# Optimization experiments

Hardware: AMD Instinct MI355X
Metric: run time of the kernel (lower is better)

The kernel has to match this reference:

```python
import jax, jax.numpy as jnp
import numpy as np

DIM = 2048
NUM_HEADS = 16
NUM_KV_HEADS = 4
HEAD_DIM = DIM // NUM_HEADS  # 128
ROPE_DIMS = HEAD_DIM         # rope_dims=0 -> full head_dim
ROPE_BASE = 10000.0
EPS = jnp.finfo(jnp.float32).eps  # torch F.rms_norm default eps


def _rms_norm(x):
    # F.rms_norm over last dim, no learned weight
    return x * jax.lax.rsqrt(jnp.mean(x * x, axis=-1, keepdims=True) + EPS)


def _rope_cos_sin(seq_len, dtype):
    inv_freq = 1.0 / (ROPE_BASE ** (jnp.arange(0, ROPE_DIMS, 2, dtype=jnp.float32) / ROPE_DIMS))
    t = jnp.arange(seq_len, dtype=jnp.float32)
    freqs = jnp.outer(t, inv_freq)  # [S, rope_dims/2]
    return jnp.cos(freqs).astype(dtype), jnp.sin(freqs).astype(dtype)


def _apply_rotary(x, cos, sin):
    # x: [B, H, S, hd]; cos/sin: [S, rope_dims/2] broadcast over B,H
    half = ROPE_DIMS // 2
    x1, x2 = x[..., :half], x[..., half:ROPE_DIMS]
    x_pass = x[..., ROPE_DIMS:]
    rotated = jnp.concatenate((x1 * cos + x2 * sin, -x1 * sin + x2 * cos), axis=-1)
    return jnp.concatenate((rotated, x_pass), axis=-1) if x_pass.shape[-1] else rotated


def setup_inputs() -> dict:
    key = jax.random.key(0)
    ks = jax.random.split(key, 6)
    B, S = 2, 2048
    kv_dim = NUM_KV_HEADS * HEAD_DIM
    scale = 0.02
    return {
        "x": jax.random.normal(ks[0], (B, S, DIM), dtype=jnp.float32),
        "Wq": jax.random.normal(ks[1], (DIM, DIM), dtype=jnp.float32) * scale,
        "Wk": jax.random.normal(ks[2], (kv_dim, DIM), dtype=jnp.float32) * scale,
        "Wv": jax.random.normal(ks[3], (kv_dim, DIM), dtype=jnp.float32) * scale,
        "Wproj": jax.random.normal(ks[4], (DIM, DIM), dtype=jnp.float32) * scale,
        "q_gain": jnp.full((NUM_HEADS,), 1.0, dtype=jnp.float32),
    }


def reference(x, Wq, Wk, Wv, Wproj, q_gain):
    B, S, D = x.shape
    H, KV, hd = NUM_HEADS, NUM_KV_HEADS, HEAD_DIM
    group = H // KV

    # QKV projections (Linear: y = x @ W.T)
    q = (x @ Wq.T).reshape(B, S, H, hd).transpose(0, 2, 1, 3)    # [B,H,S,hd]
    k = (x @ Wk.T).reshape(B, S, KV, hd).transpose(0, 2, 1, 3)   # [B,KV,S,hd]
    v = (x @ Wv.T).reshape(B, S, KV, hd).transpose(0, 2, 1, 3)

    # Per-head RMSNorm on q/k
    q = _rms_norm(q)
    k = _rms_norm(k)

    # RoPE
    cos, sin = _rope_cos_sin(S, q.dtype)
    q = _apply_rotary(q, cos, sin)
    k = _apply_rotary(k, cos, sin)

    # Per-head gain on q
    q = q * q_gain[None, :, None, None]

    # GQA: expand kv heads to H
    k = jnp.repeat(k, group, axis=1)  # [B,H,S,hd]
    v = jnp.repeat(v, group, axis=1)

    # Causal SDPA
    sm_scale = 1.0 / np.sqrt(hd)
    scores = jnp.einsum('bhqd,bhkd->bhqk', q, k) * sm_scale
    causal = jnp.tril(jnp.ones((S, S), dtype=bool))
    scores = jnp.where(causal, scores, -jnp.inf)
    attn = jax.nn.softmax(scores, axis=-1)
    y = jnp.einsum('bhqk,bhkd->bhqd', attn, v)

    y = y.transpose(0, 2, 1, 3).reshape(B, S, D)
    return y @ Wproj.T
```

## Files before the change

kernel.cpp:

```cpp
#include <hip/hip_runtime.h>
#include <hip/hip_bf16.h>
#include <stdint.h>

namespace {

constexpr int kB = 2;
constexpr int kS = 2048;
constexpr int kD = 2048;
constexpr int kH = 16;
constexpr int kKV = 4;
constexpr int kHd = 128;
constexpr int kM = kB * kS;
constexpr int kQKN = kD + kKV * kHd;

using bf = __bf16;
typedef bf bf16x8 __attribute__((ext_vector_type(8)));
typedef float f32x4 __attribute__((ext_vector_type(4)));
typedef float f32x16 __attribute__((ext_vector_type(16)));

__device__ __forceinline__ f32x4 mfma16(bf16x8 a, bf16x8 b, f32x4 c) {
  return __builtin_amdgcn_mfma_f32_16x16x32_bf16(a, b, c, 0, 0, 0);
}
__device__ __forceinline__ f32x16 mfma32(bf16x8 a, bf16x8 b, f32x16 c) {
  return __builtin_amdgcn_mfma_f32_32x32x16_bf16(a, b, c, 0, 0, 0);
}

__device__ __forceinline__ void gload_lds16(const bf* g, bf* l) {
  __builtin_amdgcn_global_load_lds(
      (const __attribute__((address_space(1))) void*)(uintptr_t)g,
      (__attribute__((address_space(3))) void*)l, 16, 0, 0);
}

__global__ __launch_bounds__(256) void cvt_all(
    const float* __restrict__ x, const float* __restrict__ wq,
    const float* __restrict__ wk, const float* __restrict__ wv,
    const float* __restrict__ wp, bf* __restrict__ xb,
    bf* __restrict__ wqkvb, bf* __restrict__ wpb) {
  int i = blockIdx.x * 256 + threadIdx.x;
  const float* src; bf* dst; int off;
  if (i < 2097152)      { src = x;  dst = xb;    off = i; }
  else if (i < 3145728) { src = wq; dst = wqkvb; off = i - 2097152; }
  else if (i < 3407872) { src = wk; dst = wqkvb + (size_t)kD * kD;               off = i - 3145728; }
  else if (i < 3670016) { src = wv; dst = wqkvb + (size_t)kD * kD + 512 * kD;    off = i - 3407872; }
  else                  { src = wp; dst = wpb;   off = i - 3670016; }
  float4 v = reinterpret_cast<const float4*>(src)[off];
  union { bf h[4]; uint2 u; } o;
  o.h[0] = (bf)v.x; o.h[1] = (bf)v.y; o.h[2] = (bf)v.z; o.h[3] = (bf)v.w;
  reinterpret_cast<uint2*>(dst)[off] = o.u;
}

template <typename CT, int TM>
__global__ __launch_bounds__(256) void gemm_bt(const bf* __restrict__ A, int lda,
                                               const bf* __restrict__ Bm, int ldb,
                                               CT* __restrict__ C, int ldc, int K) {
  __shared__ bf As[TM * 64];
  __shared__ bf Bs[128 * 64];
  const int tid = threadIdx.x;
  const int w = tid >> 6, lane = tid & 63;
  const int r16 = lane & 15, kg = lane >> 4;
  const int nwg = gridDim.x * gridDim.y;
  const int bid = blockIdx.y * gridDim.x + blockIdx.x;
  const int swz = (bid & 7) * (nwg >> 3) + (bid >> 3);
  const int bx = swz % gridDim.x, by = swz / gridDim.x;
  const int bm = by * TM, bn = bx * 128;
  const int wy = (w >> 1) * (TM / 2), wx = (w & 1) * 64;
  constexpr int MF = TM / 32;
  f32x4 acc[MF][4] = {};
  for (int kt = 0; kt < K; kt += 64) {
    __syncthreads();
#pragma unroll
    for (int r = 0; r < MF; r++) {
      int u = r * 256 + tid;
      int row = u >> 3;
      int cb = ((u & 7) * 16) ^ ((row & 7) << 4);
      gload_lds16(A + (size_t)(bm + row) * lda + kt + (cb >> 1),
                  As + (size_t)(r * 256 + w * 64) * 8);
    }
#pragma unroll
    for (int r = 0; r < 4; r++) {
      int u = r * 256 + tid;
      int row = u >> 3;
      int cb = ((u & 7) * 16) ^ ((row & 7) << 4);
      gload_lds16(Bm + (size_t)(bn + row) * ldb + kt + (cb >> 1),
                  Bs + (size_t)(r * 256 + w * 64) * 8);
    }
    __syncthreads();
#pragma unroll
    for (int ks = 0; ks < 2; ks++) {
      bf16x8 af[MF], bfr[4];
#pragma unroll
      for (int m = 0; m < MF; m++) {
        int row = wy + m * 16 + r16;
        af[m] = *reinterpret_cast<const bf16x8*>(
            reinterpret_cast<const char*>(As) + row * 128 +
            ((ks * 64 + kg * 16) ^ ((row & 7) << 4)));
      }
#pragma unroll
      for (int n = 0; n < 4; n++) {
        int row = wx + n * 16 + r16;
        bfr[n] = *reinterpret_cast<const bf16x8*>(
            reinterpret_cast<const char*>(Bs) + row * 128 +
            ((ks * 64 + kg * 16) ^ ((row & 7) << 4)));
      }
#pragma unroll
      for (int m = 0; m < MF; m++)
#pragma unroll
        for (int n = 0; n < 4; n++)
          acc[m][n] = mfma16(af[m], bfr[n], acc[m][n]);
    }
  }
#pragma unroll
  for (int m = 0; m < MF; m++)
#pragma unroll
    for (int n = 0; n < 4; n++)
#pragma unroll
      for (int r = 0; r < 4; r++) {
        int row = bm + wy + m * 16 + kg * 4 + r;
        int col = bn + wx + n * 16 + r16;
        C[(size_t)row * ldc + col] = (CT)acc[m][n][r];
      }
}

__global__ __launch_bounds__(256) void normrope(bf* __restrict__ qk,
                                                const float* __restrict__ qgain) {
  const int tid = threadIdx.x;
  const int w = tid >> 6, lane = tid & 63;
  int v = blockIdx.x * 4 + w;
  int b = v / (kS * (kH + kKV));
  int rem = v % (kS * (kH + kKV));
  int s = rem / (kH + kKV);
  int j = rem % (kH + kKV);
  int colbase = (j < kH) ? j * kHd : kD + (j - kH) * kHd;
  size_t base = (size_t)(b * kS + s) * kQKN + colbase;
  float e1 = (float)qk[base + lane];
  float e2 = (float)qk[base + 64 + lane];
  float ss = e1 * e1 + e2 * e2;
#pragma unroll
  for (int m = 1; m < 64; m <<= 1) ss += __shfl_xor(ss, m);
  float inv = rsqrtf(ss * (1.0f / 128.0f) + 1.1920929e-7f);
  e1 *= inv; e2 *= inv;
  float invfreq = exp2f((float)lane * -0.20762050593046013f);
  float ang = (float)s * invfreq;
  float sn, cs;
  sincosf(ang, &sn, &cs);
  float o1 = e1 * cs + e2 * sn;
  float o2 = -e1 * sn + e2 * cs;
  if (j < kH) {
    float g = qgain[j] * (0.08838834764831845f * 1.4426950408889634f);
    o1 *= g; o2 *= g;
  }
  qk[base + lane] = (bf)o1;
  qk[base + 64 + lane] = (bf)o2;
}

__global__ __launch_bounds__(256, 2) void attn_kernel(const bf* __restrict__ qk,
                                                      const bf* __restrict__ vt,
                                                      bf* __restrict__ y) {
  __shared__ bf Ks[2][64 * 128];
  __shared__ bf Vs[2][128 * 64];
  __shared__ float Ml[2][64][2];
  const int tid = threadIdx.x;
  const int w = tid >> 6, lane = tid & 63;
  const int q32 = lane & 31, hi = lane >> 5;
  const int qhalf = w & 1, kvhalf = w >> 1;
  const int bh = blockIdx.x;
  const int pairIdx = blockIdx.y;
  const int b = bh >> 4, h = bh & 15, kvh = h >> 2;
  const size_t rowbase = (size_t)b * kS;
  const bf* kbase = qk + kD + kvh * kHd;
  const bf* vbase = vt + (size_t)(kvh * kHd) * kM + b * kS;

  const bf* gK[4]; const bf* gV[4];
#pragma unroll
  for (int r = 0; r < 4; r++) {
    int u = r * 256 + tid;
    int krow = u >> 4, c16 = u & 15;
    gK[r] = kbase + (size_t)(rowbase + krow) * kQKN +
            (((c16 * 16) ^ ((krow & 7) << 4)) >> 1);
    int vrow = u >> 3, c8 = u & 7;
    gV[r] = vbase + (size_t)vrow * kM +
            (((c8 * 16) ^ ((vrow & 7) << 4)) >> 1);
  }

  auto stage = [&](int buf, int kt) {
    const size_t ko = (size_t)kt * (size_t)(64 * kQKN);
    const int vo = kt * 64;
#pragma unroll
    for (int r = 0; r < 4; r++)
      gload_lds16(gK[r] + ko, Ks[buf] + (size_t)(r * 256 + w * 64) * 8);
#pragma unroll
    for (int r = 0; r < 4; r++)
      gload_lds16(gV[r] + vo, Vs[buf] + (size_t)(r * 256 + w * 64) * 8);
  };

#pragma unroll 1
  for (int ph = 0; ph < 2; ph++) {
    const int j = ph ? (31 - pairIdx) : pairIdx;
    const int q0 = j * 64;
    const int qg0 = q0 + qhalf * 32;
    const int qrow = qg0 + q32;
    const int kvoff = kvhalf * 32;

    bf16x8 qf[8];
#pragma unroll
    for (int dc = 0; dc < 8; dc++)
      qf[dc] = *reinterpret_cast<const bf16x8*>(
          qk + (rowbase + qrow) * kQKN + h * kHd + dc * 16 + hi * 8);

    f32x16 o[4] = {};
    float mrun = -1e30f, lrun = 0.f;

    int cur = 0;
    stage(0, 0);

    for (int kt = 0; kt <= j; kt++) {
      asm volatile("s_barrier" ::: "memory");
      if (kt < j) {
        stage(cur ^ 1, kt + 1);
        asm volatile("s_waitcnt vmcnt(8)" ::: "memory");
      } else {
        asm volatile("s_waitcnt vmcnt(0)" ::: "memory");
      }
      asm volatile("s_barrier" ::: "memory");

      if (kt * 64 + kvoff <= qg0 + 31) {
        f32x16 sf = {};
        const int krow = kvoff + q32;
        const char* ksrow = reinterpret_cast<const char*>(Ks[cur]) + krow * 256;
        const int kswz = (krow & 7) << 4;
        __builtin_amdgcn_s_setprio(1);
#pragma unroll
        for (int dc = 0; dc < 8; dc++) {
          bf16x8 kf = *reinterpret_cast<const bf16x8*>(
              ksrow + ((dc * 32 + hi * 16) ^ kswz));
          sf = mfma32(kf, qf[dc], sf);
        }
        __builtin_amdgcn_s_setprio(0);

        if (kt * 64 + kvoff + 31 > qg0) {
#pragma unroll
          for (int r = 0; r < 16; r++) {
            int kgl = kt * 64 + kvoff + (r & 3) + 8 * (r >> 2) + 4 * hi;
            sf[r] = (kgl <= qrow) ? sf[r] : -1e30f;
          }
        }

        float rmax = sf[0];
#pragma unroll
        for (int r = 1; r < 16; r++) rmax = fmaxf(rmax, sf[r]);
        rmax = fmaxf(rmax, __shfl_xor(rmax, 32));

        if (!__all(rmax <= mrun + 8.0f)) {
          float mnew = fmaxf(mrun, rmax);
          float resc = exp2f(mrun - mnew);
          mrun = mnew;
          lrun *= resc;
          float rq[16];
#pragma unroll
          for (int r = 0; r < 16; r++)
            rq[r] = __shfl(resc, (r & 3) + 8 * (r >> 2) + 4 * hi);
#pragma unroll
          for (int db = 0; db < 4; db++)
#pragma unroll
            for (int r = 0; r < 16; r++) o[db][r] *= rq[r];
        }

        float rsum = 0.f;
#pragma unroll
        for (int r = 0; r < 16; r++) {
          float p = exp2f(sf[r] - mrun);
          sf[r] = p;
          rsum += p;
        }
        rsum += __shfl_xor(rsum, 32);
        lrun += rsum;

        bf16x8 pa[2];
        {
          uint32_t wa[4], wb[4];
#pragma unroll
          for (int g = 0; g < 4; g++) {
            asm("v_cvt_pk_bf16_f32 %0, %1, %2"
                : "=v"(wa[g]) : "v"(sf[4 * g + 0]), "v"(sf[4 * g + 1]));
            asm("v_cvt_pk_bf16_f32 %0, %1, %2"
                : "=v"(wb[g]) : "v"(sf[4 * g + 2]), "v"(sf[4 * g + 3]));
          }
          asm volatile("v_permlane32_swap_b32 %0, %1" : "+v"(wa[0]), "+v"(wa[1]));
          asm volatile("v_permlane32_swap_b32 %0, %1" : "+v"(wb[0]), "+v"(wb[1]));
          asm volatile("v_permlane32_swap_b32 %0, %1" : "+v"(wa[2]), "+v"(wa[3]));
          asm volatile("v_permlane32_swap_b32 %0, %1" : "+v"(wb[2]), "+v"(wb[3]));
          union { uint32_t u[4]; bf16x8 v; } p0, p1;
          p0.u[0] = wa[0]; p0.u[1] = wb[0]; p0.u[2] = wa[1]; p0.u[3] = wb[1];
          p1.u[0] = wa[2]; p1.u[1] = wb[2]; p1.u[2] = wa[3]; p1.u[3] = wb[3];
          pa[0] = p0.v; pa[1] = p1.v;
        }

        __builtin_amdgcn_s_setprio(1);
#pragma unroll
        for (int c = 0; c < 2; c++)
#pragma unroll
          for (int db = 0; db < 4; db++) {
            int vrow = db * 32 + q32;
            bf16x8 vb = *reinterpret_cast<const bf16x8*>(
                reinterpret_cast<const char*>(Vs[cur]) + vrow * 128 +
                ((kvhalf * 64 + c * 32 + hi * 16) ^ ((vrow & 7) << 4)));
            o[db] = mfma32(pa[c], vb, o[db]);
          }
        __builtin_amdgcn_s_setprio(0);
      }
      cur ^= 1;
    }

    __syncthreads();
    float* mb = reinterpret_cast<float*>(Ks);
    if (w >= 2) {
      Ml[w - 2][lane][0] = mrun;
      Ml[w - 2][lane][1] = lrun;
      int base = (w - 2) * 4096;
#pragma unroll
      for (int db = 0; db < 4; db++)
#pragma unroll
        for (int r = 0; r < 16; r++)
          mb[base + (db * 16 + r) * 64 + lane] = o[db][r];
    }
    __syncthreads();
    if (w < 2) {
      float m1 = Ml[w][lane][0], l1 = Ml[w][lane][1];
      float m = fmaxf(mrun, m1);
      float f0 = exp2f(mrun - m), f1 = exp2f(m1 - m);
      float linv = 1.0f / (lrun * f0 + l1 * f1);
      float av = f0 * linv, bv = f1 * linv;
      float aq[16], bq[16];
#pragma unroll
      for (int r = 0; r < 16; r++) {
        int cr = (r & 3) + 8 * (r >> 2) + 4 * hi;
        aq[r] = __shfl(av, cr);
        bq[r] = __shfl(bv, cr);
      }
      int base = w * 4096;
#pragma unroll
      for (int db = 0; db < 4; db++)
#pragma unroll
        for (int r = 0; r < 16; r++) {
          float pv = mb[base + (db * 16 + r) * 64 + lane];
          float res = o[db][r] * aq[r] + pv * bq[r];
          int s = qg0 + (r & 3) + 8 * (r >> 2) + 4 * hi;
          int d = db * 32 + q32;
          y[(rowbase + s) * kD + h * kHd + d] = (bf)res;
        }
    }
    __syncthreads();
  }
}

}

extern "C" void kernel_launch(void* const* d_in, const int* in_sizes, int n_in,
                              void* d_out, int out_size, void* d_ws, size_t ws_size,
                              hipStream_t stream) {
  const float* x  = (const float*)d_in[0];
  const float* Wq = (const float*)d_in[1];
  const float* Wk = (const float*)d_in[2];
  const float* Wv = (const float*)d_in[3];
  const float* Wp = (const float*)d_in[4];
  const float* qg = (const float*)d_in[5];

  bf* xb    = (bf*)d_ws;
  bf* wqkvb = xb + (size_t)kM * kD;
  bf* wpb   = wqkvb + (size_t)3072 * kD;
  bf* qkbuf = wpb + (size_t)kD * kD;
  bf* vtbuf = qkbuf + (size_t)kM * kQKN;
  bf* yb    = vtbuf + (size_t)512 * kM;

  cvt_all<<<18432, 256, 0, stream>>>(x, Wq, Wk, Wv, Wp, xb, wqkvb, wpb);

  gemm_bt<bf, 128><<<dim3(kQKN / 128, kM / 128), 256, 0, stream>>>(
      xb, kD, wqkvb, kD, qkbuf, kQKN, kD);

  gemm_bt<bf, 64><<<dim3(kM / 128, 512 / 64), 256, 0, stream>>>(
      wqkvb + (size_t)(kD + 512) * kD, kD, xb, kD, vtbuf, kM, kD);

  normrope<<<(kB * kS * (kH + kKV)) / 4, 256, 0, stream>>>(qkbuf, qg);

  attn_kernel<<<dim3(kB * kH, 16), 256, 0, stream>>>(qkbuf, vtbuf, yb);

  gemm_bt<float, 128><<<dim3(kD / 128, kM / 128), 256, 0, stream>>>(
      yb, kD, wpb, kD, (float*)d_out, kD, kD);
}
```

Baseline: 222.0 us.

## Load V fragments directly from global into registers and raise occupancy

Removes the LDS double buffer for V in the attention kernel. Each wave now loads its V MFMA operands straight from global memory into registers per KV tile, while K is still staged through LDS. Freeing that LDS allows launch bounds of 3 blocks per SM instead of 2. The explicit vmcnt pipelining is replaced with __syncthreads. The cost is redundant V reads across waves and global-load latency that is no longer hidden by prefetch, since the V loads are issued in the same iteration they are consumed.

```diff
diff --git a/kernel.cpp b/kernel.cpp
--- a/kernel.cpp
+++ b/kernel.cpp
@@ -153,11 +153,10 @@
   qk[base + 64 + lane] = (bf)o2;
 }
 
-__global__ __launch_bounds__(256, 2) void attn_kernel(const bf* __restrict__ qk,
+__global__ __launch_bounds__(256, 3) void attn_kernel(const bf* __restrict__ qk,
                                                       const bf* __restrict__ vt,
                                                       bf* __restrict__ y) {
   __shared__ bf Ks[2][64 * 128];
-  __shared__ bf Vs[2][128 * 64];
   __shared__ float Ml[2][64][2];
   const int tid = threadIdx.x;
   const int w = tid >> 6, lane = tid & 63;
@@ -170,27 +169,24 @@
   const bf* kbase = qk + kD + kvh * kHd;
   const bf* vbase = vt + (size_t)(kvh * kHd) * kM + b * kS;
 
-  const bf* gK[4]; const bf* gV[4];
+  const bf* gK[4];
 #pragma unroll
   for (int r = 0; r < 4; r++) {
     int u = r * 256 + tid;
     int krow = u >> 4, c16 = u & 15;
     gK[r] = kbase + (size_t)(rowbase + krow) * kQKN +
             (((c16 * 16) ^ ((krow & 7) << 4)) >> 1);
-    int vrow = u >> 3, c8 = u & 7;
-    gV[r] = vbase + (size_t)vrow * kM +
-            (((c8 * 16) ^ ((vrow & 7) << 4)) >> 1);
   }
-
-  auto stage = [&](int buf, int kt) {
+  const bf* vf[4];
+#pragma unroll
+  for (int db = 0; db < 4; db++)
+    vf[db] = vbase + (size_t)(db * 32 + q32) * kM + kvhalf * 32 + hi * 8;
+
+  auto stageK = [&](int buf, int kt) {
     const size_t ko = (size_t)kt * (size_t)(64 * kQKN);
-    const int vo = kt * 64;
 #pragma unroll
     for (int r = 0; r < 4; r++)
       gload_lds16(gK[r] + ko, Ks[buf] + (size_t)(r * 256 + w * 64) * 8);
-#pragma unroll
-    for (int r = 0; r < 4; r++)
-      gload_lds16(gV[r] + vo, Vs[buf] + (size_t)(r * 256 + w * 64) * 8);
   };
 
 #pragma unroll 1
@@ -211,19 +207,20 @@
     float mrun = -1e30f, lrun = 0.f;
 
     int cur = 0;
-    stage(0, 0);
+    stageK(0, 0);
 
     for (int kt = 0; kt <= j; kt++) {
-      asm volatile("s_barrier" ::: "memory");
-      if (kt < j) {
-        stage(cur ^ 1, kt + 1);
-        asm volatile("s_waitcnt vmcnt(8)" ::: "memory");
-      } else {
-        asm volatile("s_waitcnt vmcnt(0)" ::: "memory");
-      }
-      asm volatile("s_barrier" ::: "memory");
+      __syncthreads();
+      if (kt < j) stageK(cur ^ 1, kt + 1);
 
       if (kt * 64 + kvoff <= qg0 + 31) {
+        bf16x8 vr0[4], vr1[4];
+#pragma unroll
+        for (int db = 0; db < 4; db++) {
+          vr0[db] = *reinterpret_cast<const bf16x8*>(vf[db] + kt * 64);
+          vr1[db] = *reinterpret_cast<const bf16x8*>(vf[db] + kt * 64 + 16);
+        }
+
         f32x16 sf = {};
         const int krow = kvoff + q32;
         const char* ksrow = reinterpret_cast<const char*>(Ks[cur]) + krow * 256;
@@ -297,15 +294,10 @@
 
         __builtin_amdgcn_s_setprio(1);
 #pragma unroll
-        for (int c = 0; c < 2; c++)
-#pragma unroll
-          for (int db = 0; db < 4; db++) {
-            int vrow = db * 32 + q32;
-            bf16x8 vb = *reinterpret_cast<const bf16x8*>(
-                reinterpret_cast<const char*>(Vs[cur]) + vrow * 128 +
-                ((kvhalf * 64 + c * 32 + hi * 16) ^ ((vrow & 7) << 4)));
-            o[db] = mfma32(pa[c], vb, o[db]);
-          }
+        for (int db = 0; db < 4; db++) {
+          o[db] = mfma32(pa[0], vr0[db], o[db]);
+          o[db] = mfma32(pa[1], vr1[db], o[db]);
+        }
         __builtin_amdgcn_s_setprio(0);
       }
       cur ^= 1;
```

Measured after the change: 379.8 us. 71.1% more time.
